# Kernel optimization log

Measured on AMD Instinct MI355X. Metric: run time of the kernel, lower is better.

## Reference

```python
import jax, jax.numpy as jnp
import numpy as np

B, T, C, H = 4, 2048, 1024, 16
HD = C // H  # head_dim = 64


def setup_inputs() -> dict:
    key = jax.random.key(0)
    k1, k2, k3, k4, k5 = jax.random.split(key, 5)
    s = 1.0 / np.sqrt(C)
    return {
        "x": jax.random.normal(k1, (B, T, C), dtype=jnp.float32),
        "Wqkv": jax.random.normal(k2, (C, 3 * C), dtype=jnp.float32) * s,
        "bqkv": jnp.zeros((3 * C,), dtype=jnp.float32),
        "Wproj": jax.random.normal(k3, (C, C), dtype=jnp.float32) * s,
        "bproj": jnp.zeros((C,), dtype=jnp.float32),
    }


def reference(x, Wqkv, bqkv, Wproj, bproj):
    b, t, c = x.shape
    qkv = x @ Wqkv + bqkv                      # [B,T,3C]
    q, k, v = jnp.split(qkv, 3, axis=-1)
    # [B,T,C] -> [B,H,T,HD]
    q = q.reshape(b, t, H, HD).transpose(0, 2, 1, 3)
    k = k.reshape(b, t, H, HD).transpose(0, 2, 1, 3)
    v = v.reshape(b, t, H, HD).transpose(0, 2, 1, 3)
    att = jnp.einsum("bhqd,bhkd->bhqk", q, k) * (1.0 / np.sqrt(HD))
    causal = jnp.tril(jnp.ones((t, t), dtype=bool))
    att = jnp.where(causal[None, None], att, -jnp.inf)
    att = jax.nn.softmax(att, axis=-1)
    # dropout p=0.0 (eval) -> identity
    y = jnp.einsum("bhqk,bhkd->bhqd", att, v)  # [B,H,T,HD]
    y = y.transpose(0, 2, 1, 3).reshape(b, t, c)
    return y @ Wproj + bproj
```

## Files before the change

### kernel.cpp

```cpp
#include <hip/hip_runtime.h>


typedef unsigned short u16;
typedef short short8_t __attribute__((ext_vector_type(8)));
typedef float f32x4 __attribute__((ext_vector_type(4)));

#define B_ 4
#define T_ 2048
#define C_ 1024
#define H_ 16
#define HD_ 64

__device__ __forceinline__ u16 f32_to_bf16(float f) {
  unsigned int u = __float_as_uint(f);
  u += 0x7fffu + ((u >> 16) & 1u);
  return (u16)(u >> 16);
}

__device__ __forceinline__ void async_copy16(const void* g, void* l) {
  __builtin_amdgcn_global_load_lds((const __attribute__((address_space(1))) void*)g,
                                   (__attribute__((address_space(3))) void*)l, 16, 0, 0);
}

__global__ void cast_x_kernel(const float* __restrict__ in, u16* __restrict__ out) {
  int i = blockIdx.x * 256 + threadIdx.x;
  float4 v = ((const float4*)in)[i];
  unsigned int a = (unsigned int)f32_to_bf16(v.x) | ((unsigned int)f32_to_bf16(v.y) << 16);
  unsigned int b = (unsigned int)f32_to_bf16(v.z) | ((unsigned int)f32_to_bf16(v.w) << 16);
  ((uint2*)out)[i] = make_uint2(a, b);
}

__global__ void transpose_cast_kernel(const float* __restrict__ in, u16* __restrict__ out,
                                      int K, int N) {
  __shared__ float tile[32][33];
  int nb = blockIdx.x * 32, kb = blockIdx.y * 32;
  int c = threadIdx.x & 31, r0 = threadIdx.x >> 5;
#pragma unroll
  for (int rr = 0; rr < 4; ++rr) {
    int r = r0 + rr * 8;
    tile[r][c] = in[(size_t)(kb + r) * N + nb + c];
  }
  __syncthreads();
#pragma unroll
  for (int rr = 0; rr < 4; ++rr) {
    int r = r0 + rr * 8;
    out[(size_t)(nb + r) * K + kb + c] = f32_to_bf16(tile[c][r]);
  }
}

__device__ __forceinline__ void stage_tile(const u16* __restrict__ A, const u16* __restrict__ Bt,
                                           int K, int m0, int n0, int k0, char* buf, int tid) {
#pragma unroll
  for (int it = 0; it < 2; ++it) {
    int j = it * 256 + tid;
    int row = j >> 2;
    int ch = ((j & 3) ^ (row >> 1)) & 3;
    async_copy16(A + (size_t)(m0 + row) * K + k0 + ch * 8, buf + j * 16);
    async_copy16(Bt + (size_t)(n0 + row) * K + k0 + ch * 8, buf + 8192 + j * 16);
  }
}

__device__ __forceinline__ void gemm_mainloop(const u16* __restrict__ A, const u16* __restrict__ Bt,
                                              int K, int m0, int n0, char* smem,
                                              f32x4 (&acc)[4][4]) {
  int tid = threadIdx.x;
  int lane = tid & 63, wave = tid >> 6;
  int quad = lane >> 4, l15 = lane & 15;
  int waveM = wave >> 1, waveN = wave & 1;
  stage_tile(A, Bt, K, m0, n0, 0, smem, tid);
  int nIter = K >> 5;
  for (int ki = 0; ki < nIter; ++ki) {
    int cur = ki & 1;
    char* bufc = smem + cur * 16384;
    __syncthreads();
    if (ki + 1 < nIter)
      stage_tile(A, Bt, K, m0, n0, (ki + 1) << 5, smem + (cur ^ 1) * 16384, tid);
    short8_t af[4], bfr[4];
#pragma unroll
    for (int mt = 0; mt < 4; ++mt) {
      int row = waveM * 64 + mt * 16 + l15;
      af[mt] = *(const short8_t*)(bufc + row * 64 + (((quad ^ (row >> 1)) & 3) << 4));
    }
#pragma unroll
    for (int nt = 0; nt < 4; ++nt) {
      int row = waveN * 64 + nt * 16 + l15;
      bfr[nt] = *(const short8_t*)(bufc + 8192 + row * 64 + (((quad ^ (row >> 1)) & 3) << 4));
    }
#pragma unroll
    for (int mt = 0; mt < 4; ++mt)
#pragma unroll
      for (int nt = 0; nt < 4; ++nt)
        acc[mt][nt] = __builtin_amdgcn_mfma_f32_16x16x32_bf16(af[mt], bfr[nt], acc[mt][nt], 0, 0, 0);
  }
}

__global__ __launch_bounds__(256, 2) void gemm1_kernel(const u16* __restrict__ A,
                                                       const u16* __restrict__ Bt,
                                                       const float* __restrict__ bias,
                                                       u16* __restrict__ Qo, u16* __restrict__ Ko,
                                                       u16* __restrict__ Vo) {
  __shared__ __align__(128) char smem[32768];
  f32x4 acc[4][4];
#pragma unroll
  for (int mt = 0; mt < 4; ++mt)
#pragma unroll
    for (int nt = 0; nt < 4; ++nt) acc[mt][nt] = (f32x4){0.f, 0.f, 0.f, 0.f};
  int m0 = blockIdx.y * 128, n0 = blockIdx.x * 128;
  gemm_mainloop(A, Bt, C_, m0, n0, smem, acc);

  int lane = threadIdx.x & 63, wave = threadIdx.x >> 6;
  int quad = lane >> 4, l15 = lane & 15;
  int waveM = wave >> 1, waveN = wave & 1;

  if (n0 < 2048) {
#pragma unroll
    for (int nt = 0; nt < 4; ++nt) {
      int n = n0 + waveN * 64 + nt * 16;
      int which = n >> 10;
      int rem = n & 1023;
      int head = rem >> 6;
      int d = (rem & 63) + l15;
      float bv = bias[n + l15];
      u16* dst = (which == 0) ? Qo : Ko;
#pragma unroll
      for (int mt = 0; mt < 4; ++mt) {
#pragma unroll
        for (int r = 0; r < 4; ++r) {
          int token = m0 + waveM * 64 + mt * 16 + quad * 4 + r;
          int b = token >> 11, t = token & 2047;
          dst[(((size_t)(b * H_ + head)) * T_ + t) * HD_ + d] = f32_to_bf16(acc[mt][nt][r] + bv);
        }
      }
    }
  } else {
    __syncthreads();
    char* W = smem + wave * 8192;
#pragma unroll
    for (int nt = 0; nt < 4; ++nt) {
      int nl = nt * 16 + l15;
      float bv = bias[n0 + waveN * 64 + nl];
#pragma unroll
      for (int mt = 0; mt < 4; ++mt) {
        int g = mt * 4 + quad;
        int pc = ((g >> 1) ^ (nl & 7)) & 7;
        uint2 pv;
        pv.x = (unsigned int)f32_to_bf16(acc[mt][nt][0] + bv) |
               ((unsigned int)f32_to_bf16(acc[mt][nt][1] + bv) << 16);
        pv.y = (unsigned int)f32_to_bf16(acc[mt][nt][2] + bv) |
               ((unsigned int)f32_to_bf16(acc[mt][nt][3] + bv) << 16);
        *(uint2*)(W + nl * 128 + pc * 16 + (g & 1) * 8) = pv;
      }
    }
    int b = m0 >> 11;
#pragma unroll
    for (int i = 0; i < 8; ++i) {
      int jj = i * 64 + lane;
      int nl = jj >> 3;
      int c = jj & 7;
      int pc = c ^ (nl & 7);
      uint4 v = *(const uint4*)(W + nl * 128 + pc * 16);
      int rem = (n0 - 2048) + waveN * 64 + nl;
      int head = rem >> 6, dd = rem & 63;
      int t0 = (m0 & 2047) + waveM * 64 + c * 8;
      *(uint4*)(Vo + ((size_t)(b * H_ + head) * HD_ + dd) * T_ + t0) = v;
    }
  }
}

__global__ __launch_bounds__(256, 2) void gemm2_kernel(const u16* __restrict__ A,
                                                       const u16* __restrict__ Bt,
                                                       const float* __restrict__ bias,
                                                       float* __restrict__ out) {
  __shared__ __align__(128) char smem[32768];
  f32x4 acc[4][4];
#pragma unroll
  for (int mt = 0; mt < 4; ++mt)
#pragma unroll
    for (int nt = 0; nt < 4; ++nt) acc[mt][nt] = (f32x4){0.f, 0.f, 0.f, 0.f};
  int m0 = blockIdx.y * 128, n0 = blockIdx.x * 128;
  gemm_mainloop(A, Bt, C_, m0, n0, smem, acc);

  int lane = threadIdx.x & 63, wave = threadIdx.x >> 6;
  int quad = lane >> 4, l15 = lane & 15;
  int waveM = wave >> 1, waveN = wave & 1;
#pragma unroll
  for (int nt = 0; nt < 4; ++nt) {
    int col = n0 + waveN * 64 + nt * 16 + l15;
    float bv = bias[col];
#pragma unroll
    for (int mt = 0; mt < 4; ++mt) {
#pragma unroll
      for (int r = 0; r < 4; ++r) {
        int token = m0 + waveM * 64 + mt * 16 + quad * 4 + r;
        out[(size_t)token * C_ + col] = acc[mt][nt][r] + bv;
      }
    }
  }
}

__device__ __forceinline__ void stage_kv(const u16* __restrict__ Kb, const u16* __restrict__ Vb,
                                         int kt, char* Ksb, char* Vsb, int tid) {
#pragma unroll
  for (int it = 0; it < 2; ++it) {
    int j = it * 256 + tid;
    int row = j >> 3;
    int ch = (j & 7) ^ (row & 7);
    async_copy16(Kb + (size_t)(kt * 64 + row) * HD_ + ch * 8, Ksb + j * 16);
    async_copy16(Vb + (size_t)row * T_ + kt * 64 + ch * 8, Vsb + j * 16);
  }
}

__global__ __launch_bounds__(256, 2) void attn_kernel(const u16* __restrict__ Qg,
                                                      const u16* __restrict__ Kg,
                                                      const u16* __restrict__ Vg,
                                                      u16* __restrict__ Yg) {
  __shared__ __align__(128) char smem[65536];
  char* Qs = smem;

  int tid = threadIdx.x;
  int wave = tid >> 6, lane = tid & 63;
  int quad = lane >> 4, l15 = lane & 15;
  char* Psw = smem + 49152 + wave * 4096;
  int bh = blockIdx.x;
  int qt = 15 - blockIdx.y;
  int b = bh >> 4, h = bh & 15;
  const u16* Qb = Qg + (size_t)bh * T_ * HD_ + (size_t)qt * 128 * HD_;
  const u16* Kb = Kg + (size_t)bh * T_ * HD_;
  const u16* Vb = Vg + (size_t)bh * HD_ * T_;

#pragma unroll
  for (int it = 0; it < 4; ++it) {
    int j = it * 256 + tid;
    int row = j >> 3;
    int ch = (j & 7) ^ (row & 7);
    async_copy16(Qb + row * HD_ + ch * 8, Qs + j * 16);
  }
  stage_kv(Kb, Vb, 0, smem + 16384, smem + 32768, tid);

  float l_part[2][4];
  f32x4 o[2][4];
#pragma unroll
  for (int mt = 0; mt < 2; ++mt)
#pragma unroll
    for (int r = 0; r < 4; ++r) l_part[mt][r] = 0.f;
#pragma unroll
  for (int mt = 0; mt < 2; ++mt)
#pragma unroll
    for (int dt = 0; dt < 4; ++dt) o[mt][dt] = (f32x4){0.f, 0.f, 0.f, 0.f};

  int ktmax = 2 * qt + 1;
  for (int kt = 0; kt <= ktmax; ++kt) {
    int cur = kt & 1;
    char* Ksc = smem + 16384 + cur * 8192;
    char* Vtc = smem + 32768 + cur * 8192;
    __syncthreads();
    if (kt < ktmax)
      stage_kv(Kb, Vb, kt + 1, smem + 16384 + (cur ^ 1) * 8192, smem + 32768 + (cur ^ 1) * 8192,
               tid);

    f32x4 s[2][4];
#pragma unroll
    for (int mt = 0; mt < 2; ++mt)
#pragma unroll
      for (int nt = 0; nt < 4; ++nt) s[mt][nt] = (f32x4){0.f, 0.f, 0.f, 0.f};
#pragma unroll
    for (int ks = 0; ks < 2; ++ks) {
      short8_t af[2], bfr[4];
#pragma unroll
      for (int mt = 0; mt < 2; ++mt) {
        int row = wave * 32 + mt * 16 + l15;
        af[mt] = *(const short8_t*)(Qs + row * 128 + ((((ks * 4 + quad) ^ row) & 7) << 4));
      }
#pragma unroll
      for (int nt = 0; nt < 4; ++nt) {
        int row = nt * 16 + l15;
        bfr[nt] = *(const short8_t*)(Ksc + row * 128 + ((((ks * 4 + quad) ^ row) & 7) << 4));
      }
#pragma unroll
      for (int mt = 0; mt < 2; ++mt)
#pragma unroll
        for (int nt = 0; nt < 4; ++nt)
          s[mt][nt] = __builtin_amdgcn_mfma_f32_16x16x32_bf16(af[mt], bfr[nt], s[mt][nt], 0, 0, 0);
    }

    bool domask = (kt >= 2 * qt);
#pragma unroll
    for (int mt = 0; mt < 2; ++mt) {
      int qrow0 = qt * 128 + wave * 32 + mt * 16 + quad * 4;
#pragma unroll
      for (int nt = 0; nt < 4; ++nt) {
        int col = kt * 64 + nt * 16 + l15;
#pragma unroll
        for (int r = 0; r < 4; ++r) {
          float p = __expf(s[mt][nt][r] * 0.125f);
          if (domask && col > qrow0 + r) p = 0.f;
          s[mt][nt][r] = p;
        }
      }
#pragma unroll
      for (int r = 0; r < 4; ++r)
        l_part[mt][r] += (s[mt][0][r] + s[mt][1][r]) + (s[mt][2][r] + s[mt][3][r]);
#pragma unroll
      for (int nt = 0; nt < 4; ++nt) {
        int col = nt * 16 + l15;
#pragma unroll
        for (int r = 0; r < 4; ++r) {
          int prow = mt * 16 + quad * 4 + r;
          *(u16*)(Psw + prow * 128 + ((((col >> 3) ^ prow) & 7) << 4) + ((col & 7) << 1)) =
              (u16)(__float_as_uint(s[mt][nt][r]) >> 16);
        }
      }
    }

#pragma unroll
    for (int ks = 0; ks < 2; ++ks) {
      short8_t af[2], bfr[4];
#pragma unroll
      for (int mt = 0; mt < 2; ++mt) {
        int row = mt * 16 + l15;
        af[mt] = *(const short8_t*)(Psw + row * 128 + ((((ks * 4 + quad) ^ row) & 7) << 4));
      }
#pragma unroll
      for (int dt = 0; dt < 4; ++dt) {
        int row = dt * 16 + l15;
        bfr[dt] = *(const short8_t*)(Vtc + row * 128 + ((((ks * 4 + quad) ^ row) & 7) << 4));
      }
#pragma unroll
      for (int mt = 0; mt < 2; ++mt)
#pragma unroll
        for (int dt = 0; dt < 4; ++dt)
          o[mt][dt] = __builtin_amdgcn_mfma_f32_16x16x32_bf16(af[mt], bfr[dt], o[mt][dt], 0, 0, 0);
    }
  }

#pragma unroll
  for (int mt = 0; mt < 2; ++mt) {
#pragma unroll
    for (int r = 0; r < 4; ++r) {
      float lsum = l_part[mt][r];
#pragma unroll
      for (int off = 1; off < 16; off <<= 1) lsum += __shfl_xor(lsum, off);
      float inv = 1.0f / lsum;
#pragma unroll
      for (int dt = 0; dt < 4; ++dt) {
        int t = qt * 128 + wave * 32 + mt * 16 + quad * 4 + r;
        float val = o[mt][dt][r] * inv;
        Yg[((size_t)(b * T_ + t)) * C_ + h * HD_ + dt * 16 + l15] = f32_to_bf16(val);
      }
    }
  }
}

extern "C" void kernel_launch(void* const* d_in, const int* in_sizes, int n_in,
                              void* d_out, int out_size, void* d_ws, size_t ws_size,
                              hipStream_t stream) {
  (void)in_sizes; (void)n_in; (void)out_size; (void)ws_size;
  const float* x = (const float*)d_in[0];
  const float* Wqkv = (const float*)d_in[1];
  const float* bqkv = (const float*)d_in[2];
  const float* Wproj = (const float*)d_in[3];
  const float* bproj = (const float*)d_in[4];
  float* out = (float*)d_out;
  char* ws = (char*)d_ws;

  u16* Xb = (u16*)ws;
  u16* WqkvT = (u16*)(ws + 16777216);
  u16* WprojT = (u16*)(ws + 16777216 + 6291456);
  u16* Q = (u16*)(ws + 25165824);
  u16* K = Q + 8388608;
  u16* V = K + 8388608;
  u16* Y = Xb;

  cast_x_kernel<<<8192, 256, 0, stream>>>(x, Xb);
  transpose_cast_kernel<<<dim3(96, 32), 256, 0, stream>>>(Wqkv, WqkvT, C_, 3 * C_);
  transpose_cast_kernel<<<dim3(32, 32), 256, 0, stream>>>(Wproj, WprojT, C_, C_);
  gemm1_kernel<<<dim3(24, 64), 256, 0, stream>>>(Xb, WqkvT, bqkv, Q, K, V);
  attn_kernel<<<dim3(64, 16), 256, 0, stream>>>(Q, K, V, Y);
  gemm2_kernel<<<dim3(8, 64), 256, 0, stream>>>(Y, WprojT, bproj, out);
}
```

Before: 255.4 us.

## Enlarge attention query tile to 256 rows with register-held Q and per-wave causal skip

The attention kernel now uses 512-thread blocks covering 256 query rows, so each staged K/V tile is shared by twice as many queries. Q fragments are loaded straight into registers instead of LDS, which frees shared memory. Waves skip key tiles beyond their own causal limit and apply masking only on their diagonal tile. The softmax scale times log2(e) is folded into Q in the QKV GEMM epilogue so the inner loop can use a bare exp2. Risks are higher register pressure, a 4-blocks-per-CU launch bound that may not be reachable, and idle waves within a block on the diagonal tiles.

```diff
diff --git a/kernel.cpp b/kernel.cpp
--- a/kernel.cpp
+++ b/kernel.cpp
@@ -10,6 +10,7 @@
 #define C_ 1024
 #define H_ 16
 #define HD_ 64
+#define QSCALE 0.18033688011112042f
 
 __device__ __forceinline__ u16 f32_to_bf16(float f) {
   unsigned int u = __float_as_uint(f);
@@ -121,6 +122,7 @@
       int head = rem >> 6;
       int d = (rem & 63) + l15;
       float bv = bias[n + l15];
+      float sc = (which == 0) ? QSCALE : 1.0f;
       u16* dst = (which == 0) ? Qo : Ko;
 #pragma unroll
       for (int mt = 0; mt < 4; ++mt) {
@@ -128,7 +130,8 @@
         for (int r = 0; r < 4; ++r) {
           int token = m0 + waveM * 64 + mt * 16 + quad * 4 + r;
           int b = token >> 11, t = token & 2047;
-          dst[(((size_t)(b * H_ + head)) * T_ + t) * HD_ + d] = f32_to_bf16(acc[mt][nt][r] + bv);
+          dst[(((size_t)(b * H_ + head)) * T_ + t) * HD_ + d] =
+              f32_to_bf16((acc[mt][nt][r] + bv) * sc);
         }
       }
     }
@@ -200,42 +203,38 @@
 
 __device__ __forceinline__ void stage_kv(const u16* __restrict__ Kb, const u16* __restrict__ Vb,
                                          int kt, char* Ksb, char* Vsb, int tid) {
-#pragma unroll
-  for (int it = 0; it < 2; ++it) {
-    int j = it * 256 + tid;
-    int row = j >> 3;
-    int ch = (j & 7) ^ (row & 7);
-    async_copy16(Kb + (size_t)(kt * 64 + row) * HD_ + ch * 8, Ksb + j * 16);
-    async_copy16(Vb + (size_t)row * T_ + kt * 64 + ch * 8, Vsb + j * 16);
-  }
-}
-
-__global__ __launch_bounds__(256, 2) void attn_kernel(const u16* __restrict__ Qg,
+  int row = tid >> 3;
+  int ch = (tid & 7) ^ (row & 7);
+  async_copy16(Kb + (size_t)(kt * 64 + row) * HD_ + ch * 8, Ksb + tid * 16);
+  async_copy16(Vb + (size_t)row * T_ + kt * 64 + ch * 8, Vsb + tid * 16);
+}
+
+__global__ __launch_bounds__(512, 4) void attn_kernel(const u16* __restrict__ Qg,
                                                       const u16* __restrict__ Kg,
                                                       const u16* __restrict__ Vg,
                                                       u16* __restrict__ Yg) {
   __shared__ __align__(128) char smem[65536];
-  char* Qs = smem;
-
   int tid = threadIdx.x;
   int wave = tid >> 6, lane = tid & 63;
   int quad = lane >> 4, l15 = lane & 15;
-  char* Psw = smem + 49152 + wave * 4096;
+  char* Psw = smem + 32768 + wave * 4096;
   int bh = blockIdx.x;
-  int qt = 15 - blockIdx.y;
+  int y = blockIdx.y;
+  int qt = (y < 4) ? (7 - y) : (y - 4);
   int b = bh >> 4, h = bh & 15;
-  const u16* Qb = Qg + (size_t)bh * T_ * HD_ + (size_t)qt * 128 * HD_;
   const u16* Kb = Kg + (size_t)bh * T_ * HD_;
   const u16* Vb = Vg + (size_t)bh * HD_ * T_;
 
-#pragma unroll
-  for (int it = 0; it < 4; ++it) {
-    int j = it * 256 + tid;
-    int row = j >> 3;
-    int ch = (j & 7) ^ (row & 7);
-    async_copy16(Qb + row * HD_ + ch * 8, Qs + j * 16);
-  }
-  stage_kv(Kb, Vb, 0, smem + 16384, smem + 32768, tid);
+  short8_t qf[2][2];
+#pragma unroll
+  for (int mt = 0; mt < 2; ++mt)
+#pragma unroll
+    for (int ks = 0; ks < 2; ++ks) {
+      int row = qt * 256 + wave * 32 + mt * 16 + l15;
+      qf[mt][ks] = *(const short8_t*)(Qg + ((size_t)bh * T_ + row) * HD_ + ks * 32 + quad * 8);
+    }
+
+  stage_kv(Kb, Vb, 0, smem, smem + 16384, tid);
 
   float l_part[2][4];
   f32x4 o[2][4];
@@ -248,15 +247,16 @@
 #pragma unroll
     for (int dt = 0; dt < 4; ++dt) o[mt][dt] = (f32x4){0.f, 0.f, 0.f, 0.f};
 
-  int ktmax = 2 * qt + 1;
-  for (int kt = 0; kt <= ktmax; ++kt) {
+  int ktmax_blk = 4 * qt + 3;
+  int ktmax_wave = 4 * qt + (wave >> 1);
+  for (int kt = 0; kt <= ktmax_blk; ++kt) {
     int cur = kt & 1;
-    char* Ksc = smem + 16384 + cur * 8192;
-    char* Vtc = smem + 32768 + cur * 8192;
+    char* Ksc = smem + cur * 8192;
+    char* Vtc = smem + 16384 + cur * 8192;
     __syncthreads();
-    if (kt < ktmax)
-      stage_kv(Kb, Vb, kt + 1, smem + 16384 + (cur ^ 1) * 8192, smem + 32768 + (cur ^ 1) * 8192,
-               tid);
+    if (kt < ktmax_blk)
+      stage_kv(Kb, Vb, kt + 1, smem + (cur ^ 1) * 8192, smem + 16384 + (cur ^ 1) * 8192, tid);
+    if (kt > ktmax_wave) continue;
 
     f32x4 s[2][4];
 #pragma unroll
@@ -265,12 +265,7 @@
       for (int nt = 0; nt < 4; ++nt) s[mt][nt] = (f32x4){0.f, 0.f, 0.f, 0.f};
 #pragma unroll
     for (int ks = 0; ks < 2; ++ks) {
-      short8_t af[2], bfr[4];
-#pragma unroll
-      for (int mt = 0; mt < 2; ++mt) {
-        int row = wave * 32 + mt * 16 + l15;
-        af[mt] = *(const short8_t*)(Qs + row * 128 + ((((ks * 4 + quad) ^ row) & 7) << 4));
-      }
+      short8_t bfr[4];
 #pragma unroll
       for (int nt = 0; nt < 4; ++nt) {
         int row = nt * 16 + l15;
@@ -280,23 +275,35 @@
       for (int mt = 0; mt < 2; ++mt)
 #pragma unroll
         for (int nt = 0; nt < 4; ++nt)
-          s[mt][nt] = __builtin_amdgcn_mfma_f32_16x16x32_bf16(af[mt], bfr[nt], s[mt][nt], 0, 0, 0);
-    }
-
-    bool domask = (kt >= 2 * qt);
+          s[mt][nt] = __builtin_amdgcn_mfma_f32_16x16x32_bf16(qf[mt][ks], bfr[nt], s[mt][nt], 0, 0, 0);
+    }
+
+    if (kt == ktmax_wave) {
+#pragma unroll
+      for (int mt = 0; mt < 2; ++mt) {
+        int qrow0 = qt * 256 + wave * 32 + mt * 16 + quad * 4;
+#pragma unroll
+        for (int nt = 0; nt < 4; ++nt) {
+          int col = kt * 64 + nt * 16 + l15;
+#pragma unroll
+          for (int r = 0; r < 4; ++r) {
+            float p = __builtin_amdgcn_exp2f(s[mt][nt][r]);
+            if (col > qrow0 + r) p = 0.f;
+            s[mt][nt][r] = p;
+          }
+        }
+      }
+    } else {
+#pragma unroll
+      for (int mt = 0; mt < 2; ++mt)
+#pragma unroll
+        for (int nt = 0; nt < 4; ++nt)
+#pragma unroll
+          for (int r = 0; r < 4; ++r) s[mt][nt][r] = __builtin_amdgcn_exp2f(s[mt][nt][r]);
+    }
+
 #pragma unroll
     for (int mt = 0; mt < 2; ++mt) {
-      int qrow0 = qt * 128 + wave * 32 + mt * 16 + quad * 4;
-#pragma unroll
-      for (int nt = 0; nt < 4; ++nt) {
-        int col = kt * 64 + nt * 16 + l15;
-#pragma unroll
-        for (int r = 0; r < 4; ++r) {
-          float p = __expf(s[mt][nt][r] * 0.125f);
-          if (domask && col > qrow0 + r) p = 0.f;
-          s[mt][nt][r] = p;
-        }
-      }
 #pragma unroll
       for (int r = 0; r < 4; ++r)
         l_part[mt][r] += (s[mt][0][r] + s[mt][1][r]) + (s[mt][2][r] + s[mt][3][r]);
@@ -343,7 +350,7 @@
       float inv = 1.0f / lsum;
 #pragma unroll
       for (int dt = 0; dt < 4; ++dt) {
-        int t = qt * 128 + wave * 32 + mt * 16 + quad * 4 + r;
+        int t = qt * 256 + wave * 32 + mt * 16 + quad * 4 + r;
         float val = o[mt][dt][r] * inv;
         Yg[((size_t)(b * T_ + t)) * C_ + h * HD_ + dt * 16 + l15] = f32_to_bf16(val);
       }
@@ -375,6 +382,6 @@
   transpose_cast_kernel<<<dim3(96, 32), 256, 0, stream>>>(Wqkv, WqkvT, C_, 3 * C_);
   transpose_cast_kernel<<<dim3(32, 32), 256, 0, stream>>>(Wproj, WprojT, C_, C_);
   gemm1_kernel<<<dim3(24, 64), 256, 0, stream>>>(Xb, WqkvT, bqkv, Q, K, V);
-  attn_kernel<<<dim3(64, 16), 256, 0, stream>>>(Q, K, V, Y);
+  attn_kernel<<<dim3(64, 8), 512, 0, stream>>>(Q, K, V, Y);
   gemm2_kernel<<<dim3(8, 64), 256, 0, stream>>>(Y, WprojT, bproj, out);
 }
```

After: 288.8 us. 1.13x slower.
